# Optimization experiments

Hardware: AMD Instinct MI355X
Metric: run time of the kernel (lower is better)

The kernel has to match this reference:

```python
import jax, jax.numpy as jnp
import numpy as np

OBS_DIM = 64; ACT_DIM = 18; INTER = 64; COMMAND = 32
UNITS = ACT_DIM + COMMAND + INTER  # 114; neuron order: [motor, command, inter]
Q_HIDDEN = max(32, UNITS)
B, T = 2048, 64
ODE_UNFOLDS = 6
EPS = 1e-8


def _build_wiring(seed=0):
    """NCP sparse wiring: sensory->inter, inter->command, command recurrent, command->motor."""
    rng = np.random.default_rng(seed)
    adj = np.zeros((UNITS, UNITS), np.float32)   # [pre, post]
    sens = np.zeros((OBS_DIM, UNITS), np.float32)
    motor = np.arange(ACT_DIM)
    cmd = np.arange(ACT_DIM, ACT_DIM + COMMAND)
    inter = np.arange(ACT_DIM + COMMAND, UNITS)
    for s in range(OBS_DIM):
        for d in rng.choice(inter, size=8, replace=False):
            sens[s, d] = rng.choice([-1.0, 1.0])
    for i in inter:
        for d in rng.choice(cmd, size=8, replace=False):
            adj[i, d] = rng.choice([-1.0, 1.0])
    for _ in range(32):
        adj[rng.choice(cmd), rng.choice(cmd)] = rng.choice([-1.0, 1.0])
    for m in motor:
        for s in rng.choice(cmd, size=8, replace=False):
            adj[s, m] = rng.choice([-1.0, 1.0])
    return adj, sens


def setup_inputs() -> dict:
    key = jax.random.key(0)
    ks = jax.random.split(key, 16)
    adj, sens = _build_wiring()
    u = lambda k, shape, lo, hi: jax.random.uniform(k, shape, jnp.float32, lo, hi)
    return {
        "obs": jax.random.normal(ks[0], (B, T, OBS_DIM), jnp.float32),
        "hidden": jnp.zeros((B, UNITS), jnp.float32),
        "input_w": jnp.ones((OBS_DIM,), jnp.float32),
        "input_b": jnp.zeros((OBS_DIM,), jnp.float32),
        "sensory_w": u(ks[1], (OBS_DIM, UNITS), 0.001, 1.0),
        "sensory_mu": u(ks[2], (OBS_DIM, UNITS), 0.3, 0.8),
        "sensory_sigma": u(ks[3], (OBS_DIM, UNITS), 3.0, 8.0),
        "sensory_erev": jnp.asarray(sens),
        "sensory_mask": jnp.asarray(np.abs(sens)),
        "w": u(ks[4], (UNITS, UNITS), 0.001, 1.0),
        "mu": u(ks[5], (UNITS, UNITS), 0.3, 0.8),
        "sigma": u(ks[6], (UNITS, UNITS), 3.0, 8.0),
        "erev": jnp.asarray(adj),
        "mask": jnp.asarray(np.abs(adj)),
        "gleak": u(ks[7], (UNITS,), 0.001, 1.0),
        "vleak": u(ks[8], (UNITS,), -0.2, 0.2),
        "cm": u(ks[9], (UNITS,), 0.4, 0.6),
        "q_w1": jax.random.normal(ks[10], (UNITS, Q_HIDDEN), jnp.float32) / np.sqrt(UNITS).astype(np.float32),
        "q_b1": jnp.zeros((Q_HIDDEN,), jnp.float32),
        "q_w2": jax.random.normal(ks[11], (Q_HIDDEN, ACT_DIM), jnp.float32) / np.sqrt(Q_HIDDEN).astype(np.float32),
        "q_b2": jnp.zeros((ACT_DIM,), jnp.float32),
    }


def _ltc_forward(obs, hidden, input_w, input_b, sensory_w, sensory_mu, sensory_sigma,
                 sensory_erev, sensory_mask, w, mu, sigma, erev, mask, gleak, vleak, cm):
    sw = sensory_w * sensory_mask          # sparse sensory synapses (S, U)
    ww = w * mask                          # sparse recurrent synapses (U, U)
    cm_t = cm * ODE_UNFOLDS                # cm / (elapsed_time / ode_unfolds), elapsed_time = 1.0

    @jax.checkpoint
    def step(h, x):
        xi = x * input_w + input_b                                                    # (B, S) affine input map
        s_act = sw * jax.nn.sigmoid((xi[:, :, None] - sensory_mu) * sensory_sigma)    # (B, S, U)
        w_num_s = jnp.sum(s_act * sensory_erev, axis=1)                               # (B, U)
        w_den_s = jnp.sum(s_act, axis=1)                                              # (B, U)

        def unfold(v, _):
            act = ww * jax.nn.sigmoid((v[:, :, None] - mu) * sigma)                   # (B, U, U)
            num = cm_t * v + gleak * vleak + jnp.sum(act * erev, axis=1) + w_num_s
            den = cm_t + gleak + jnp.sum(act, axis=1) + w_den_s
            return num / (den + EPS), None

        v, _ = jax.lax.scan(unfold, h, None, length=ODE_UNFOLDS)
        return v, None

    h, _ = jax.lax.scan(step, hidden, jnp.swapaxes(obs, 0, 1))  # scan over time
    return h


def reference(obs, hidden, input_w, input_b, sensory_w, sensory_mu, sensory_sigma,
              sensory_erev, sensory_mask, w, mu, sigma, erev, mask, gleak, vleak, cm,
              q_w1, q_b1, q_w2, q_b2):
    h = _ltc_forward(obs, hidden, input_w, input_b, sensory_w, sensory_mu, sensory_sigma,
                     sensory_erev, sensory_mask, w, mu, sigma, erev, mask, gleak, vleak, cm)
    q = jax.nn.relu(h @ q_w1 + q_b1) @ q_w2 + q_b2  # Q-head over full hidden state
    return q, h
```

## Files before the change

kernel.cpp:

```cpp
#include <hip/hip_runtime.h>

#define UNITS   114
#define SDIM    64
#define ACT     18
#define TSTEPS  64

#define CR 13
#define CS 9
#define MSTRIDE 24

#define LOG2E 1.4426950408889634f
#define EPS   1e-8f

typedef float v2f __attribute__((ext_vector_type(2)));
__device__ __forceinline__ v2f fma2(v2f a, v2f b, v2f c) {
  return __builtin_elementwise_fma(a, b, c);
}
__device__ __forceinline__ float bperm(int addr, float v) {
  return __int_as_float(__builtin_amdgcn_ds_bpermute(addr, __float_as_int(v)));
}
__device__ __forceinline__ float dperm(int addr, float v) {
  return __int_as_float(__builtin_amdgcn_ds_permute(addr, __float_as_int(v)));
}
__device__ __forceinline__ void wsync() {
  __builtin_amdgcn_fence(__ATOMIC_ACQ_REL, "wavefront");
  __builtin_amdgcn_wave_barrier();
}
__device__ __forceinline__ int canonLane(int u) { return (u >= 64) ? (u - 64) : u; }

__device__ __forceinline__ int kthSetBit(unsigned long long m, int k) {
  int pos = 0;
#pragma unroll
  for (int ww = 32; ww >= 1; ww >>= 1) {
    const unsigned long long lowMask = ((1ull << ww) - 1ull);
    const int c = __popcll(m & lowMask);
    if (k >= c) { k -= c; m >>= ww; pos += ww; }
  }
  return pos;
}
__device__ __forceinline__ unsigned long long shfl_u64(unsigned long long v, int src) {
  const int lo = __shfl((int)(unsigned)(v & 0xffffffffull), src);
  const int hi = __shfl((int)(unsigned)(v >> 32), src);
  return ((unsigned long long)(unsigned)hi << 32) | (unsigned)lo;
}

__global__ __launch_bounds__(64) void build_all(
    const float* __restrict__ w,  const float* __restrict__ mu,
    const float* __restrict__ sigma, const float* __restrict__ erev,
    const float* __restrict__ mask,
    const float* __restrict__ sw, const float* __restrict__ smu,
    const float* __restrict__ ssg, const float* __restrict__ serev,
    const float* __restrict__ smask,
    float4* __restrict__ recP4, float2* __restrict__ recP2, int* __restrict__ recAd,
    float4* __restrict__ senP4, float2* __restrict__ senP2, int* __restrict__ senAd,
    int* __restrict__ meta)
{
  const int l = threadIdx.x;
  const int bid = blockIdx.x;
  __shared__ int degL[64], pF0L[64];
  __shared__ int contIdx[64], contOwn[64], splitRole[64], split2[64], ownP[128];
  __shared__ int rcv[64];

  contIdx[l] = 0; contOwn[l] = 0; splitRole[l] = -1; split2[l] = 0;
  ownP[2*l] = -1; ownP[2*l+1] = -1;

  if (bid < 4) {
    unsigned long long cLo = 0ull, cHi = 0ull;
    if (l < 50) {
      for (int base = 0; base < 64; base += 16) {
        float mv[16];
#pragma unroll
        for (int q = 0; q < 16; ++q) mv[q] = mask[(18 + base + q)*UNITS + l];
#pragma unroll
        for (int q = 0; q < 16; ++q) if (mv[q] != 0.f) cLo |= (1ull << (base + q));
      }
      for (int base = 0; base < 32; base += 16) {
        float mv[16];
#pragma unroll
        for (int q = 0; q < 16; ++q) mv[q] = mask[(82 + base + q)*UNITS + l];
#pragma unroll
        for (int q = 0; q < 16; ++q) if (mv[q] != 0.f) cHi |= (1ull << (base + q));
      }
    }
    const int dreg = __popcll(cLo) + __popcll(cHi);
    degL[l] = dreg;
    wsync();
    {
      int lam = 0, f = 0, pc = 0;
      for (int p = 0; p < 50; ++p) {
        const int dd = __shfl(dreg, p);
        if (pc == 2 || f == CR || dd > 3*CR - f) { ++lam; f = 0; pc = 0; }
        if (lam > 63) lam = 63;
        if (l == 0) { pF0L[p] = f; ownP[2*lam + pc] = p; }
        const int owner = lam, role = pc; ++pc;
        const int take = dd < (CR - f) ? dd : (CR - f);
        f += take; int rem = dd - take;
        if (rem > 0) {
          if (l == 0) { splitRole[owner] = role; split2[owner] = (rem > CR) ? 1 : 0; }
          ++lam; if (lam > 63) lam = 63;
          if (l == 0) { contIdx[lam] = 1; contOwn[lam] = owner; }
          pc = 1;
          const int t2 = rem < CR ? rem : CR; f = t2; rem -= t2;
          if (rem > 0) {
            ++lam; if (lam > 63) lam = 63;
            if (l == 0) { contIdx[lam] = 2; contOwn[lam] = owner; }
            pc = 1; f = rem;
          }
        }
      }
    }
    wsync();
    int dAr = (contIdx[l] == 1) ? contOwn[l] : -1;
    int dBr = (contIdx[l] == 2) ? contOwn[l] : -1;
    rcv[l] = 0; wsync();
    if (dAr >= 0) rcv[dAr] = 1;
    wsync();
    { const unsigned long long rM = __ballot(rcv[l] != 0), dM = __ballot(dAr < 0);
      if (dAr < 0) dAr = kthSetBit(~rM, __popcll(dM & ((1ull << l) - 1ull))); }
    wsync();
    rcv[l] = 0; wsync();
    if (dBr >= 0) rcv[dBr] = 1;
    wsync();
    { const unsigned long long rM = __ballot(rcv[l] != 0), dM = __ballot(dBr < 0);
      if (dBr < 0) dBr = kthSetBit(~rM, __popcll(dM & ((1ull << l) - 1ull))); }
    const int uA = ownP[2*l], uB = ownP[2*l+1];
    if (bid == 0) {
      int* M = meta + l * MSTRIDE;
      M[0] = dAr * 4; M[1] = dBr * 4;
      const float s1A = (splitRole[l] == 0) ? 1.f : 0.f, s1B = (splitRole[l] == 1) ? 1.f : 0.f;
      M[2] = __float_as_int(s1A); M[3] = __float_as_int(s1B);
      const float s2 = split2[l] ? 1.f : 0.f;
      M[4] = __float_as_int(s1A * s2); M[5] = __float_as_int(s1B * s2);
      M[6] = ((uA >= 0) ? uA : 128 + l) * 4;
      M[7] = ((uB >= 0) ? uB : 192 + l) * 4;
      M[8] = (uA >= 0) ? uA : 0;
      M[9] = (uB >= 0) ? uB : 0;
    }
    const int ci = contIdx[l];
    int p1 = -1, br = 0, cnt1 = 0;
    if (ci) {
      const int o = contOwn[l];
      p1 = ownP[2*o + splitRole[o]];
      br = (CR - pF0L[p1]) + ((ci == 2) ? CR : 0);
      cnt1 = degL[p1] - br; if (cnt1 > CR) cnt1 = CR;
    }
    int fA = 0, tA = -1;
    if (uA >= 0) { fA = pF0L[uA]; const int rm = CR - fA; const int dd = degL[uA]; tA = dd < rm ? dd : rm; }
    int fB = 0, tB = -1;
    if (uB >= 0) { fB = pF0L[uB]; const int rm = CR - fB; const int dd = degL[uB]; tB = dd < rm ? dd : rm; }
    for (int s = bid; s < CR; s += 4) {
      int post = -1, rank = 0, isB = 0;
      if (ci && s < cnt1)                          { post = p1; rank = br + s; }
      else if (uA >= 0 && s >= fA && s < fA + tA)  { post = uA; rank = s - fA; }
      else if (uB >= 0 && s >= fB && s < fB + tB)  { post = uB; rank = s - fB; isB = 1; }
      const int postc = (post >= 0) ? post : 0;
      const unsigned long long plo = shfl_u64(cLo, postc);
      const unsigned long long phi = shfl_u64(cHi, postc);
      float4 p4 = make_float4(0.f, 0.f, 0.f, 0.f);
      float2 p2 = make_float2(0.f, 0.f);
      int ad = 0;
      if (post >= 0) {
        const int c = __popcll(plo);
        const int pre = (rank < c) ? (18 + kthSetBit(plo, rank)) : (82 + kthSetBit(phi, rank - c));
        const int idx = pre * UNITS + post;
        const float sg_ = sigma[idx];
        const float nsgl = -sg_ * LOG2E, msl = mu[idx] * sg_ * LOG2E;
        const float wd = w[idx], wn = wd * erev[idx];
        p4 = make_float4(nsgl, msl, isB ? 0.f : wn, isB ? 0.f : wd);
        p2 = isB ? make_float2(wn, wd) : make_float2(0.f, 0.f);
        ad = pre * 4;
      }
      recP4[s*64 + l] = p4; recP2[s*64 + l] = p2; recAd[s*64 + l] = ad;
    }
  } else {
    unsigned long long cS = 0ull;
    {
      const int col = 50 + l;
      for (int base = 0; base < 64; base += 16) {
        float mv[16];
#pragma unroll
        for (int q = 0; q < 16; ++q) mv[q] = smask[(base + q)*UNITS + col];
#pragma unroll
        for (int q = 0; q < 16; ++q) if (mv[q] != 0.f) cS |= (1ull << (base + q));
      }
    }
    const int dreg = __popcll(cS);
    degL[l] = dreg;
    wsync();
    {
      int lam = 0, f = 0, pc = 0;
      for (int p = 0; p < 64; ++p) {
        const int dd = __shfl(dreg, p);
        if (pc == 2 || f == CS || dd > 3*CS - f) { ++lam; f = 0; pc = 0; }
        if (lam > 63) lam = 63;
        if (l == 0) { pF0L[p] = f; ownP[2*lam + pc] = p; }
        const int owner = lam, role = pc; ++pc;
        const int take = dd < (CS - f) ? dd : (CS - f);
        f += take; int rem = dd - take;
        if (rem > 0) {
          if (l == 0) { splitRole[owner] = role; split2[owner] = (rem > CS) ? 1 : 0; }
          ++lam; if (lam > 63) lam = 63;
          if (l == 0) { contIdx[lam] = 1; contOwn[lam] = owner; }
          pc = 1;
          const int t2 = rem < CS ? rem : CS; f = t2; rem -= t2;
          if (rem > 0) {
            ++lam; if (lam > 63) lam = 63;
            if (l == 0) { contIdx[lam] = 2; contOwn[lam] = owner; }
            pc = 1; f = rem;
          }
        }
      }
    }
    wsync();
    int dAs = (contIdx[l] == 1) ? contOwn[l] : -1;
    int dBs = (contIdx[l] == 2) ? contOwn[l] : -1;
    rcv[l] = 0; wsync();
    if (dAs >= 0) rcv[dAs] = 1;
    wsync();
    { const unsigned long long rM = __ballot(rcv[l] != 0), dM = __ballot(dAs < 0);
      if (dAs < 0) dAs = kthSetBit(~rM, __popcll(dM & ((1ull << l) - 1ull))); }
    wsync();
    rcv[l] = 0; wsync();
    if (dBs >= 0) rcv[dBs] = 1;
    wsync();
    { const unsigned long long rM = __ballot(rcv[l] != 0), dM = __ballot(dBs < 0);
      if (dBs < 0) dBs = kthSetBit(~rM, __popcll(dM & ((1ull << l) - 1ull))); }
    wsync();
    int rAs = (ownP[2*l]   >= 0) ? canonLane(50 + ownP[2*l])   : -1;
    int rBs = (ownP[2*l+1] >= 0) ? canonLane(50 + ownP[2*l+1]) : -1;
    rcv[l] = 0; wsync();
    if (rAs >= 0) rcv[rAs] = 1;
    wsync();
    const int isRcvA = rcv[l];
    { const unsigned long long rM = __ballot(isRcvA != 0), dM = __ballot(rAs < 0);
      if (rAs < 0) rAs = kthSetBit(~rM, __popcll(dM & ((1ull << l) - 1ull))); }
    wsync();
    rcv[l] = 0; wsync();
    if (rBs >= 0) rcv[rBs] = 1;
    wsync();
    { const unsigned long long rM = __ballot(rcv[l] != 0), dM = __ballot(rBs < 0);
      if (rBs < 0) rBs = kthSetBit(~rM, __popcll(dM & ((1ull << l) - 1ull))); }
    const int pAs = ownP[2*l], pBs = ownP[2*l+1];
    if (bid == 4) {
      int* M = meta + l * MSTRIDE;
      M[10] = dAs * 4; M[11] = dBs * 4;
      const float s1A = (splitRole[l] == 0) ? 1.f : 0.f, s1B = (splitRole[l] == 1) ? 1.f : 0.f;
      M[12] = __float_as_int(s1A); M[13] = __float_as_int(s1B);
      const float s2 = split2[l] ? 1.f : 0.f;
      M[14] = __float_as_int(s1A * s2); M[15] = __float_as_int(s1B * s2);
      M[16] = rAs * 4; M[17] = rBs * 4;
      M[18] = __float_as_int(isRcvA ? 1.f : 0.f);
      M[19] = __float_as_int(isRcvA ? 0.f : 1.f);
      M[20] = (pAs >= 0) ? 50 + pAs : 0;
      M[21] = (pBs >= 0) ? 50 + pBs : 0;
    }
    const int ci = contIdx[l];
    int p1 = -1, br = 0, cnt1 = 0;
    if (ci) {
      const int o = contOwn[l];
      p1 = ownP[2*o + splitRole[o]];
      br = (CS - pF0L[p1]) + ((ci == 2) ? CS : 0);
      cnt1 = degL[p1] - br; if (cnt1 > CS) cnt1 = CS;
    }
    int fA = 0, tA = -1;
    if (pAs >= 0) { fA = pF0L[pAs]; const int rm = CS - fA; const int dd = degL[pAs]; tA = dd < rm ? dd : rm; }
    int fB = 0, tB = -1;
    if (pBs >= 0) { fB = pF0L[pBs]; const int rm = CS - fB; const int dd = degL[pBs]; tB = dd < rm ? dd : rm; }
    for (int s = bid - 4; s < CS; s += 4) {
      int post = -1, rank = 0, isB = 0;
      if (ci && s < cnt1)                            { post = p1;  rank = br + s; }
      else if (pAs >= 0 && s >= fA && s < fA + tA)   { post = pAs; rank = s - fA; }
      else if (pBs >= 0 && s >= fB && s < fB + tB)   { post = pBs; rank = s - fB; isB = 1; }
      const int postc = (post >= 0) ? post : 0;
      const unsigned long long pm = shfl_u64(cS, postc);
      float4 p4 = make_float4(0.f, 0.f, 0.f, 0.f);
      float2 p2 = make_float2(0.f, 0.f);
      int ad = 0;
      if (post >= 0) {
        const int pre = kthSetBit(pm, rank);
        const int idx = pre * UNITS + 50 + post;
        const float sg_ = ssg[idx];
        const float nsgl = -sg_ * LOG2E, msl = smu[idx] * sg_ * LOG2E;
        const float wd = sw[idx], wn = wd * serev[idx];
        p4 = make_float4(nsgl, msl, isB ? 0.f : wn, isB ? 0.f : wd);
        p2 = isB ? make_float2(wn, wd) : make_float2(0.f, 0.f);
        ad = pre * 4;
      }
      senP4[s*64 + l] = p4; senP2[s*64 + l] = p2; senAd[s*64 + l] = ad;
    }
  }
}

__global__ __launch_bounds__(64, 2) void ltc_run(
    const float* __restrict__ obs,     const float* __restrict__ hidden,
    const float* __restrict__ input_w, const float* __restrict__ input_b,
    const float* __restrict__ gleak,   const float* __restrict__ vleak,
    const float* __restrict__ cm,
    const float* __restrict__ q_w1, const float* __restrict__ q_b1,
    const float* __restrict__ q_w2, const float* __restrict__ q_b2,
    const float4* __restrict__ recP4, const float2* __restrict__ recP2,
    const int* __restrict__ recAd,
    const float4* __restrict__ senP4, const float2* __restrict__ senP2,
    const int* __restrict__ senAd,
    const int* __restrict__ meta, float* __restrict__ out, int B)
{
  const int l = threadIdx.x, b = blockIdx.x;
  __shared__ float mirror[256];
  char* mbase = (char*)mirror;

  float rNS[CR], rMS[CR]; v2f rWA[CR], rWB[CR]; int rad[CR];
#pragma unroll
  for (int s = 0; s < CR; ++s) {
    const float4 p4 = recP4[s*64 + l]; const float2 p2 = recP2[s*64 + l];
    rNS[s] = p4.x; rMS[s] = p4.y; rWA[s] = (v2f){p4.z, p4.w};
    rWB[s] = (v2f){p2.x, p2.y}; rad[s] = recAd[s*64 + l];
  }
  float sNS[CS], sMS[CS]; v2f sWA[CS], sWB[CS]; int sad[CS];
#pragma unroll
  for (int s = 0; s < CS; ++s) {
    const float4 p4 = senP4[s*64 + l]; const float2 p2 = senP2[s*64 + l];
    sNS[s] = p4.x; sMS[s] = p4.y; sWA[s] = (v2f){p4.z, p4.w};
    sWB[s] = (v2f){p2.x, p2.y}; sad[s] = senAd[s*64 + l];
  }

  const int* M = meta + l * MSTRIDE;
  const int   rPush1 = M[0], rPush2 = M[1];
  const v2f gR1A = {__int_as_float(M[2]), __int_as_float(M[2])};
  const v2f gR1B = {__int_as_float(M[3]), __int_as_float(M[3])};
  const v2f gR2A = {__int_as_float(M[4]), __int_as_float(M[4])};
  const v2f gR2B = {__int_as_float(M[5]), __int_as_float(M[5])};
  const int   rWrA = M[6], rWrB = M[7], rUA = M[8], rUB = M[9];
  const int   sPush1 = M[10], sPush2 = M[11];
  const v2f gS1A = {__int_as_float(M[12]), __int_as_float(M[12])};
  const v2f gS1B = {__int_as_float(M[13]), __int_as_float(M[13])};
  const v2f gS2A = {__int_as_float(M[14]), __int_as_float(M[14])};
  const v2f gS2B = {__int_as_float(M[15]), __int_as_float(M[15])};
  const int   sRtA = M[16], sRtB = M[17];
  const float sRndA = __int_as_float(M[18]), sRndB = __int_as_float(M[19]);
  const int   sUA = M[20], sUB = M[21];

  const float cmA  = cm[rUA]*6.f, glvA  = gleak[rUA]*vleak[rUA], cgA  = cm[rUA]*6.f + gleak[rUA] + EPS;
  const float cmB  = cm[rUB]*6.f, glvB  = gleak[rUB]*vleak[rUB], cgB  = cm[rUB]*6.f + gleak[rUB] + EPS;
  const float cmSA = cm[sUA]*6.f, glvSA = gleak[sUA]*vleak[sUA], cgSA = cm[sUA]*6.f + gleak[sUA] + EPS;
  const float cmSB = cm[sUB]*6.f, glvSB = gleak[sUB]*vleak[sUB], cgSB = cm[sUB]*6.f + gleak[sUB] + EPS;

  const bool ownA  = (rWrA < 512), ownB  = (rWrB < 512);
  const bool ownSA = (sUA != 0),   ownSB = (sUB != 0);
  const v2f initRA = ownA  ? (v2f){glvA,  cgA}  : (v2f){0.f, EPS};
  const v2f initRB = ownB  ? (v2f){glvB,  cgB}  : (v2f){0.f, EPS};
  const v2f initSA = ownSA ? (v2f){glvSA, cgSA} : (v2f){0.f, EPS};
  const v2f initSB = ownSB ? (v2f){glvSB, cgSB} : (v2f){0.f, EPS};

  const int  iUnit = (l < 50) ? 64 + l : l;
  const int  iWr   = iUnit * 4;
  float vIn = hidden[(size_t)b*UNITS + iUnit];
  float vPA = hidden[(size_t)b*UNITS + rUA];
  float vPB = hidden[(size_t)b*UNITS + rUB];

  mirror[l] = hidden[(size_t)b*UNITS + l];
  if (l < 50) mirror[64 + l] = hidden[(size_t)b*UNITS + 64 + l];

  const float iw = input_w[l], ibv = input_b[l];
  const float* ob = obs + (size_t)b*(TSTEPS*SDIM) + l;

  float aI, bI;
  {
    const float xi = fmaf(ob[0], iw, ibv);
    float uu[CS];
#pragma unroll
    for (int s = 0; s < CS; ++s) {
      float z = fmaf(bperm(sad[s], xi), sNS[s], sMS[s]);
      z = fminf(z, 30.f);
      uu[s] = 1.f + __builtin_amdgcn_exp2f(z);
    }
    float sg[CS];
#pragma unroll
    for (int q = 0; q < 4; ++q) {
      const float p = uu[2*q] * uu[2*q+1];
      const float r = __builtin_amdgcn_rcpf(p);
      sg[2*q]   = uu[2*q+1] * r;
      sg[2*q+1] = uu[2*q]   * r;
    }
    sg[8] = __builtin_amdgcn_rcpf(uu[8]);
    v2f cA = {0.f,0.f}, cB = {0.f,0.f};
#pragma unroll
    for (int s = 0; s < CS; ++s) {
      const v2f s2 = {sg[s], sg[s]};
      cA = fma2(sWA[s], s2, cA);
      cB = fma2(sWB[s], s2, cB);
    }
    const v2f m1 = {dperm(sPush1, cA.x), dperm(sPush1, cA.y)};
    const v2f m2 = {dperm(sPush2, cA.x), dperm(sPush2, cA.y)};
    v2f tA = fma2(gS1A, m1, cA); tA = fma2(gS2A, m2, tA);
    v2f tB = fma2(gS1B, m1, cB); tB = fma2(gS2B, m2, tB);
    const float rdA = __builtin_amdgcn_rcpf(cgSA + tA.y);
    const float aA = cmSA * rdA, bA = (glvSA + tA.x) * rdA;
    const float rdB = __builtin_amdgcn_rcpf(cgSB + tB.y);
    const float aB = cmSB * rdB, bB = (glvSB + tB.x) * rdB;
    const float ra1 = dperm(sRtA, aA), rb1 = dperm(sRtA, bA);
    const float ra2 = dperm(sRtB, aB), rb2 = dperm(sRtB, bB);
    aI = sRndA*ra1 + sRndB*ra2;
    bI = sRndA*rb1 + sRndB*rb2;
  }

  float xiN = fmaf(ob[SDIM], iw, ibv);
  float xrC = ob[2*SDIM];
  float su[CS];
  v2f acA = initSA, acB = initSB;
  v2f tSA = {0.f,0.f}, tSB = {0.f,0.f};
  float aIn = 0.f, bIn = 0.f;

  auto unfold = [&](auto chunk) {
    wsync();
    float uu[CR];
#pragma unroll
    for (int s = 0; s < CR; ++s) {
      const float pv = *(const float*)(mbase + rad[s]);
      const float z = fmaf(pv, rNS[s], rMS[s]);
      uu[s] = 1.f + __builtin_amdgcn_exp2f(z);
    }
    chunk();
    float sg[CR];
#pragma unroll
    for (int q = 0; q < 5; ++q) {
      const float p = uu[2*q] * uu[2*q+1];
      const float r = __builtin_amdgcn_rcpf(p);
      sg[2*q]   = uu[2*q+1] * r;
      sg[2*q+1] = uu[2*q]   * r;
    }
    {
      const float p01 = uu[10]*uu[11];
      const float r = __builtin_amdgcn_rcpf(p01*uu[12]);
      const float t12 = uu[12]*r;
      sg[10] = uu[11]*t12; sg[11] = uu[10]*t12; sg[12] = p01*r;
    }
    v2f a0 = initRA, a1 = {0.f,0.f}, b0 = initRB, b1 = {0.f,0.f};
#pragma unroll
    for (int s = 0; s < CR; ++s) {
      const v2f s2 = {sg[s], sg[s]};
      if (s & 1) { a1 = fma2(rWA[s], s2, a1); b1 = fma2(rWB[s], s2, b1); }
      else       { a0 = fma2(rWA[s], s2, a0); b0 = fma2(rWB[s], s2, b0); }
    }
    v2f aA = a0 + a1, aB = b0 + b1;
    const v2f m1 = {dperm(rPush1, aA.x), dperm(rPush1, aA.y)};
    const v2f m2 = {dperm(rPush2, aA.x), dperm(rPush2, aA.y)};
    v2f tA = fma2(gR1A, m1, aA); tA = fma2(gR2A, m2, tA);
    v2f tB = fma2(gR1B, m1, aB); tB = fma2(gR2B, m2, tB);
    const float dAq = tA.y, dBq = tB.y;
    const float rr = __builtin_amdgcn_rcpf(dAq * dBq);
    vPA = fmaf(cmA, vPA, tA.x) * (dBq * rr);
    vPB = fmaf(cmB, vPB, tB.x) * (dAq * rr);
    vIn = fmaf(aI, vIn, bI);
    wsync();
    *(float*)(mbase + rWrA) = vPA;
    *(float*)(mbase + rWrB) = vPB;
    *(float*)(mbase + iWr)  = vIn;
  };

  auto sExp = [&](int s) {
    float z = fmaf(bperm(sad[s], xiN), sNS[s], sMS[s]);
    z = fminf(z, 30.f);
    su[s] = 1.f + __builtin_amdgcn_exp2f(z);
  };
  auto sPair = [&](int s0) {
    const float p = su[s0] * su[s0+1];
    const float r = __builtin_amdgcn_rcpf(p);
    const float g0 = su[s0+1] * r, g1 = su[s0] * r;
    acA = fma2(sWA[s0],   (v2f){g0,g0}, acA);
    acA = fma2(sWA[s0+1], (v2f){g1,g1}, acA);
    acB = fma2(sWB[s0],   (v2f){g0,g0}, acB);
    acB = fma2(sWB[s0+1], (v2f){g1,g1}, acB);
  };

#pragma unroll 1
  for (int t = 0; t < TSTEPS; ++t) {
    unfold([&]{ sExp(0); sExp(1); });
    unfold([&]{ sExp(2); sExp(3); sPair(0); });
    unfold([&]{ sExp(4); sExp(5); sPair(2); });
    unfold([&]{ sExp(6); sExp(7); sExp(8); sPair(4); });
    unfold([&]{
      const float p67 = su[6] * su[7];
      const float r = __builtin_amdgcn_rcpf(p67 * su[8]);
      const float t67 = su[8] * r;
      const float g6 = su[7]*t67, g7 = su[6]*t67, g8 = p67*r;
      acA = fma2(sWA[6], (v2f){g6,g6}, acA); acB = fma2(sWB[6], (v2f){g6,g6}, acB);
      acA = fma2(sWA[7], (v2f){g7,g7}, acA); acB = fma2(sWB[7], (v2f){g7,g7}, acB);
      acA = fma2(sWA[8], (v2f){g8,g8}, acA); acB = fma2(sWB[8], (v2f){g8,g8}, acB);
      const v2f m1 = {dperm(sPush1, acA.x), dperm(sPush1, acA.y)};
      const v2f m2 = {dperm(sPush2, acA.x), dperm(sPush2, acA.y)};
      tSA = fma2(gS1A, m1, acA); tSA = fma2(gS2A, m2, tSA);
      tSB = fma2(gS1B, m1, acB); tSB = fma2(gS2B, m2, tSB);
    });
    unfold([&]{
      const float dA_ = tSA.y, dB_ = tSB.y;
      const float rr = __builtin_amdgcn_rcpf(dA_ * dB_);
      const float rdA = dB_ * rr, rdB = dA_ * rr;
      const float aA = cmSA * rdA, bA = tSA.x * rdA;
      const float aB = cmSB * rdB, bB = tSB.x * rdB;
      const float ra1 = dperm(sRtA, aA), rb1 = dperm(sRtA, bA);
      const float ra2 = dperm(sRtB, aB), rb2 = dperm(sRtB, bB);
      aIn = sRndA*ra1 + sRndB*ra2;
      bIn = sRndA*rb1 + sRndB*rb2;
    });
    aI = aIn; bI = bIn;
    xiN = fmaf(xrC, iw, ibv);
    const int tn = (t + 3 < TSTEPS) ? (t + 3) : (TSTEPS - 1);
    xrC = ob[tn * SDIM];
    acA = initSA; acB = initSB;
  }
  wsync();

  float* __restrict__ outH = out + (size_t)B * ACT;
  outH[(size_t)b*UNITS + l] = mirror[l];
  if (l < 50) outH[(size_t)b*UNITS + 64 + l] = mirror[64 + l];

  const int j2 = (l < 50) ? 64 + l : l;
  float h1 = q_b1[l], h2 = q_b1[j2];
  for (int i = 0; i < UNITS; ++i) {
    const float hv = mirror[i];
    h1 = fmaf(hv, q_w1[i*UNITS + l],  h1);
    h2 = fmaf(hv, q_w1[i*UNITS + j2], h2);
  }
  h1 = fmaxf(h1, 0.f); h2 = fmaxf(h2, 0.f);
  wsync();
  mirror[l] = h1;
  if (l < 50) mirror[64 + l] = h2;
  wsync();
  if (l < ACT) {
    float q = q_b2[l];
    for (int i = 0; i < UNITS; ++i) q = fmaf(mirror[i], q_w2[i*ACT + l], q);
    out[(size_t)b*ACT + l] = q;
  }
}

extern "C" void kernel_launch(void* const* d_in, const int* in_sizes, int n_in,
                              void* d_out, int out_size, void* d_ws, size_t ws_size,
                              hipStream_t stream)
{
  const float* obs           = (const float*)d_in[0];
  const float* hidden        = (const float*)d_in[1];
  const float* input_w       = (const float*)d_in[2];
  const float* input_b       = (const float*)d_in[3];
  const float* sensory_w     = (const float*)d_in[4];
  const float* sensory_mu    = (const float*)d_in[5];
  const float* sensory_sigma = (const float*)d_in[6];
  const float* sensory_erev  = (const float*)d_in[7];
  const float* sensory_mask  = (const float*)d_in[8];
  const float* w             = (const float*)d_in[9];
  const float* mu            = (const float*)d_in[10];
  const float* sigma         = (const float*)d_in[11];
  const float* erev          = (const float*)d_in[12];
  const float* mask          = (const float*)d_in[13];
  const float* gleak         = (const float*)d_in[14];
  const float* vleak         = (const float*)d_in[15];
  const float* cm            = (const float*)d_in[16];
  const float* q_w1          = (const float*)d_in[17];
  const float* q_b1          = (const float*)d_in[18];
  const float* q_w2          = (const float*)d_in[19];
  const float* q_b2          = (const float*)d_in[20];

  char* ws = (char*)d_ws;
  float4* recP4 = (float4*)(ws);
  float2* recP2 = (float2*)(ws + 13312);
  int*    recAd = (int*)   (ws + 19968);
  float4* senP4 = (float4*)(ws + 23296);
  float2* senP2 = (float2*)(ws + 32512);
  int*    senAd = (int*)   (ws + 37120);
  int*    meta  = (int*)   (ws + 39424);

  build_all<<<8, 64, 0, stream>>>(
      w, mu, sigma, erev, mask,
      sensory_w, sensory_mu, sensory_sigma, sensory_erev, sensory_mask,
      recP4, recP2, recAd, senP4, senP2, senAd, meta);

  const int B = in_sizes[0] / (TSTEPS * SDIM);
  ltc_run<<<B, 64, 0, stream>>>(
      obs, hidden, input_w, input_b, gleak, vleak, cm,
      q_w1, q_b1, q_w2, q_b2,
      recP4, recP2, recAd, senP4, senP2, senAd, meta,
      (float*)d_out, B);
}
```

Baseline: 359.3 us.

## Split LTC recurrence across two waves with shared-memory partial sums

Each block now runs two wavefronts: the first handles 8 of the 13 recurrent synapse slots and the state update, and the second handles the remaining 5 slots plus the sensory/input pipeline, passing partial sums through shared memory. Sensory weights move from registers to LDS to reduce register pressure and allow higher occupancy. The intent is to shorten per-unfold critical-path work, at the cost of two block-level barriers per ODE unfold instead of wavefront-only syncs.

```diff
diff --git a/kernel.cpp b/kernel.cpp
--- a/kernel.cpp
+++ b/kernel.cpp
@@ -8,6 +8,9 @@
 #define CR 13
 #define CS 9
 #define MSTRIDE 24
+
+#define NR0 8
+#define NR1 (CR - NR0)
 
 #define LOG2E 1.4426950408889634f
 #define EPS   1e-8f
@@ -291,7 +294,7 @@
   }
 }
 
-__global__ __launch_bounds__(64, 2) void ltc_run(
+__global__ __launch_bounds__(128, 4) void ltc_run(
     const float* __restrict__ obs,     const float* __restrict__ hidden,
     const float* __restrict__ input_w, const float* __restrict__ input_b,
     const float* __restrict__ gleak,   const float* __restrict__ vleak,
@@ -304,232 +307,274 @@
     const int* __restrict__ senAd,
     const int* __restrict__ meta, float* __restrict__ out, int B)
 {
-  const int l = threadIdx.x, b = blockIdx.x;
+  const int tid = threadIdx.x, b = blockIdx.x, cl = tid & 63;
   __shared__ float mirror[256];
+  __shared__ float4 part[64];
+  __shared__ float4 sw4[CS*64];
   char* mbase = (char*)mirror;
 
-  float rNS[CR], rMS[CR]; v2f rWA[CR], rWB[CR]; int rad[CR];
-#pragma unroll
-  for (int s = 0; s < CR; ++s) {
-    const float4 p4 = recP4[s*64 + l]; const float2 p2 = recP2[s*64 + l];
-    rNS[s] = p4.x; rMS[s] = p4.y; rWA[s] = (v2f){p4.z, p4.w};
-    rWB[s] = (v2f){p2.x, p2.y}; rad[s] = recAd[s*64 + l];
+  if (tid < UNITS) mirror[tid] = hidden[(size_t)b*UNITS + tid];
+  for (int i = tid; i < CS*64; i += 128) {
+    const float4 p4 = senP4[i]; const float2 p2 = senP2[i];
+    sw4[i] = make_float4(p4.z, p4.w, p2.x, p2.y);
   }
-  float sNS[CS], sMS[CS]; v2f sWA[CS], sWB[CS]; int sad[CS];
-#pragma unroll
-  for (int s = 0; s < CS; ++s) {
-    const float4 p4 = senP4[s*64 + l]; const float2 p2 = senP2[s*64 + l];
-    sNS[s] = p4.x; sMS[s] = p4.y; sWA[s] = (v2f){p4.z, p4.w};
-    sWB[s] = (v2f){p2.x, p2.y}; sad[s] = senAd[s*64 + l];
-  }
-
-  const int* M = meta + l * MSTRIDE;
-  const int   rPush1 = M[0], rPush2 = M[1];
+  const int* M = meta + cl * MSTRIDE;
+  const int rPush1 = M[0], rPush2 = M[1];
   const v2f gR1A = {__int_as_float(M[2]), __int_as_float(M[2])};
   const v2f gR1B = {__int_as_float(M[3]), __int_as_float(M[3])};
   const v2f gR2A = {__int_as_float(M[4]), __int_as_float(M[4])};
   const v2f gR2B = {__int_as_float(M[5]), __int_as_float(M[5])};
-  const int   rWrA = M[6], rWrB = M[7], rUA = M[8], rUB = M[9];
-  const int   sPush1 = M[10], sPush2 = M[11];
-  const v2f gS1A = {__int_as_float(M[12]), __int_as_float(M[12])};
-  const v2f gS1B = {__int_as_float(M[13]), __int_as_float(M[13])};
-  const v2f gS2A = {__int_as_float(M[14]), __int_as_float(M[14])};
-  const v2f gS2B = {__int_as_float(M[15]), __int_as_float(M[15])};
-  const int   sRtA = M[16], sRtB = M[17];
-  const float sRndA = __int_as_float(M[18]), sRndB = __int_as_float(M[19]);
-  const int   sUA = M[20], sUB = M[21];
-
-  const float cmA  = cm[rUA]*6.f, glvA  = gleak[rUA]*vleak[rUA], cgA  = cm[rUA]*6.f + gleak[rUA] + EPS;
-  const float cmB  = cm[rUB]*6.f, glvB  = gleak[rUB]*vleak[rUB], cgB  = cm[rUB]*6.f + gleak[rUB] + EPS;
-  const float cmSA = cm[sUA]*6.f, glvSA = gleak[sUA]*vleak[sUA], cgSA = cm[sUA]*6.f + gleak[sUA] + EPS;
-  const float cmSB = cm[sUB]*6.f, glvSB = gleak[sUB]*vleak[sUB], cgSB = cm[sUB]*6.f + gleak[sUB] + EPS;
-
-  const bool ownA  = (rWrA < 512), ownB  = (rWrB < 512);
-  const bool ownSA = (sUA != 0),   ownSB = (sUB != 0);
-  const v2f initRA = ownA  ? (v2f){glvA,  cgA}  : (v2f){0.f, EPS};
-  const v2f initRB = ownB  ? (v2f){glvB,  cgB}  : (v2f){0.f, EPS};
-  const v2f initSA = ownSA ? (v2f){glvSA, cgSA} : (v2f){0.f, EPS};
-  const v2f initSB = ownSB ? (v2f){glvSB, cgSB} : (v2f){0.f, EPS};
-
-  const int  iUnit = (l < 50) ? 64 + l : l;
-  const int  iWr   = iUnit * 4;
-  float vIn = hidden[(size_t)b*UNITS + iUnit];
-  float vPA = hidden[(size_t)b*UNITS + rUA];
-  float vPB = hidden[(size_t)b*UNITS + rUB];
-
-  mirror[l] = hidden[(size_t)b*UNITS + l];
-  if (l < 50) mirror[64 + l] = hidden[(size_t)b*UNITS + 64 + l];
-
-  const float iw = input_w[l], ibv = input_b[l];
-  const float* ob = obs + (size_t)b*(TSTEPS*SDIM) + l;
-
-  float aI, bI;
-  {
-    const float xi = fmaf(ob[0], iw, ibv);
-    float uu[CS];
+  __syncthreads();
+
+  if (tid < 64) {
+    float rNS[NR0], rMS[NR0]; v2f rWA[NR0], rWB[NR0]; int rad[NR0];
+#pragma unroll
+    for (int s = 0; s < NR0; ++s) {
+      const float4 p4 = recP4[s*64 + cl]; const float2 p2 = recP2[s*64 + cl];
+      rNS[s] = p4.x; rMS[s] = p4.y; rWA[s] = (v2f){p4.z, p4.w};
+      rWB[s] = (v2f){p2.x, p2.y}; rad[s] = recAd[s*64 + cl];
+    }
+    const int rWrA = M[6], rWrB = M[7], rUA = M[8], rUB = M[9];
+    const float cmA = cm[rUA]*6.f, glvA = gleak[rUA]*vleak[rUA], cgA = cm[rUA]*6.f + gleak[rUA] + EPS;
+    const float cmB = cm[rUB]*6.f, glvB = gleak[rUB]*vleak[rUB], cgB = cm[rUB]*6.f + gleak[rUB] + EPS;
+    const bool ownA = (rWrA < 512), ownB = (rWrB < 512);
+    const v2f initRA = ownA ? (v2f){glvA, cgA} : (v2f){0.f, EPS};
+    const v2f initRB = ownB ? (v2f){glvB, cgB} : (v2f){0.f, EPS};
+    float vPA = hidden[(size_t)b*UNITS + rUA];
+    float vPB = hidden[(size_t)b*UNITS + rUB];
+
+#pragma unroll 1
+    for (int it = 0; it < TSTEPS*6; ++it) {
+      __syncthreads();
+      float uu[NR0];
+#pragma unroll
+      for (int s = 0; s < NR0; ++s) {
+        const float pv = *(const float*)(mbase + rad[s]);
+        const float z = fmaf(pv, rNS[s], rMS[s]);
+        uu[s] = 1.f + __builtin_amdgcn_exp2f(z);
+      }
+      float sg[NR0];
+#pragma unroll
+      for (int q = 0; q < NR0/2; ++q) {
+        const float p = uu[2*q] * uu[2*q+1];
+        const float r = __builtin_amdgcn_rcpf(p);
+        sg[2*q]   = uu[2*q+1] * r;
+        sg[2*q+1] = uu[2*q]   * r;
+      }
+      v2f a0 = initRA, a1 = {0.f,0.f}, b0 = initRB, b1 = {0.f,0.f};
+#pragma unroll
+      for (int s = 0; s < NR0; ++s) {
+        const v2f s2 = {sg[s], sg[s]};
+        if (s & 1) { a1 = fma2(rWA[s], s2, a1); b1 = fma2(rWB[s], s2, b1); }
+        else       { a0 = fma2(rWA[s], s2, a0); b0 = fma2(rWB[s], s2, b0); }
+      }
+      const v2f aA = a0 + a1, aB = b0 + b1;
+      const v2f m1 = {dperm(rPush1, aA.x), dperm(rPush1, aA.y)};
+      const v2f m2 = {dperm(rPush2, aA.x), dperm(rPush2, aA.y)};
+      v2f tA = fma2(gR1A, m1, aA); tA = fma2(gR2A, m2, tA);
+      v2f tB = fma2(gR1B, m1, aB); tB = fma2(gR2B, m2, tB);
+      __syncthreads();
+      const float4 pp = part[cl];
+      tA = tA + (v2f){pp.x, pp.y};
+      tB = tB + (v2f){pp.z, pp.w};
+      const float dAq = tA.y, dBq = tB.y;
+      const float rr = __builtin_amdgcn_rcpf(dAq * dBq);
+      vPA = fmaf(cmA, vPA, tA.x) * (dBq * rr);
+      vPB = fmaf(cmB, vPB, tB.x) * (dAq * rr);
+      *(float*)(mbase + rWrA) = vPA;
+      *(float*)(mbase + rWrB) = vPB;
+    }
+  } else {
+    float rNS[NR1], rMS[NR1]; v2f rWA[NR1], rWB[NR1]; int rad[NR1];
+#pragma unroll
+    for (int s = 0; s < NR1; ++s) {
+      const float4 p4 = recP4[(NR0+s)*64 + cl]; const float2 p2 = recP2[(NR0+s)*64 + cl];
+      rNS[s] = p4.x; rMS[s] = p4.y; rWA[s] = (v2f){p4.z, p4.w};
+      rWB[s] = (v2f){p2.x, p2.y}; rad[s] = recAd[(NR0+s)*64 + cl];
+    }
+    float sNS[CS], sMS[CS]; int sad[CS];
 #pragma unroll
     for (int s = 0; s < CS; ++s) {
-      float z = fmaf(bperm(sad[s], xi), sNS[s], sMS[s]);
-      z = fminf(z, 30.f);
-      uu[s] = 1.f + __builtin_amdgcn_exp2f(z);
-    }
-    float sg[CS];
-#pragma unroll
-    for (int q = 0; q < 4; ++q) {
-      const float p = uu[2*q] * uu[2*q+1];
-      const float r = __builtin_amdgcn_rcpf(p);
-      sg[2*q]   = uu[2*q+1] * r;
-      sg[2*q+1] = uu[2*q]   * r;
-    }
-    sg[8] = __builtin_amdgcn_rcpf(uu[8]);
-    v2f cA = {0.f,0.f}, cB = {0.f,0.f};
-#pragma unroll
-    for (int s = 0; s < CS; ++s) {
-      const v2f s2 = {sg[s], sg[s]};
-      cA = fma2(sWA[s], s2, cA);
-      cB = fma2(sWB[s], s2, cB);
-    }
-    const v2f m1 = {dperm(sPush1, cA.x), dperm(sPush1, cA.y)};
-    const v2f m2 = {dperm(sPush2, cA.x), dperm(sPush2, cA.y)};
-    v2f tA = fma2(gS1A, m1, cA); tA = fma2(gS2A, m2, tA);
-    v2f tB = fma2(gS1B, m1, cB); tB = fma2(gS2B, m2, tB);
-    const float rdA = __builtin_amdgcn_rcpf(cgSA + tA.y);
-    const float aA = cmSA * rdA, bA = (glvSA + tA.x) * rdA;
-    const float rdB = __builtin_amdgcn_rcpf(cgSB + tB.y);
-    const float aB = cmSB * rdB, bB = (glvSB + tB.x) * rdB;
-    const float ra1 = dperm(sRtA, aA), rb1 = dperm(sRtA, bA);
-    const float ra2 = dperm(sRtB, aB), rb2 = dperm(sRtB, bB);
-    aI = sRndA*ra1 + sRndB*ra2;
-    bI = sRndA*rb1 + sRndB*rb2;
-  }
-
-  float xiN = fmaf(ob[SDIM], iw, ibv);
-  float xrC = ob[2*SDIM];
-  float su[CS];
-  v2f acA = initSA, acB = initSB;
-  v2f tSA = {0.f,0.f}, tSB = {0.f,0.f};
-  float aIn = 0.f, bIn = 0.f;
-
-  auto unfold = [&](auto chunk) {
-    wsync();
-    float uu[CR];
-#pragma unroll
-    for (int s = 0; s < CR; ++s) {
-      const float pv = *(const float*)(mbase + rad[s]);
-      const float z = fmaf(pv, rNS[s], rMS[s]);
-      uu[s] = 1.f + __builtin_amdgcn_exp2f(z);
-    }
-    chunk();
-    float sg[CR];
-#pragma unroll
-    for (int q = 0; q < 5; ++q) {
-      const float p = uu[2*q] * uu[2*q+1];
-      const float r = __builtin_amdgcn_rcpf(p);
-      sg[2*q]   = uu[2*q+1] * r;
-      sg[2*q+1] = uu[2*q]   * r;
-    }
+      const float4 p4 = senP4[s*64 + cl];
+      sNS[s] = p4.x; sMS[s] = p4.y; sad[s] = senAd[s*64 + cl];
+    }
+    const int sPush1 = M[10], sPush2 = M[11];
+    const v2f gS1A = {__int_as_float(M[12]), __int_as_float(M[12])};
+    const v2f gS1B = {__int_as_float(M[13]), __int_as_float(M[13])};
+    const v2f gS2A = {__int_as_float(M[14]), __int_as_float(M[14])};
+    const v2f gS2B = {__int_as_float(M[15]), __int_as_float(M[15])};
+    const int sRtA = M[16], sRtB = M[17];
+    const float sRndA = __int_as_float(M[18]), sRndB = __int_as_float(M[19]);
+    const int sUA = M[20], sUB = M[21];
+    const float cmSA = cm[sUA]*6.f, glvSA = gleak[sUA]*vleak[sUA], cgSA = cm[sUA]*6.f + gleak[sUA] + EPS;
+    const float cmSB = cm[sUB]*6.f, glvSB = gleak[sUB]*vleak[sUB], cgSB = cm[sUB]*6.f + gleak[sUB] + EPS;
+    const bool ownSA = (sUA != 0), ownSB = (sUB != 0);
+    const v2f initSA = ownSA ? (v2f){glvSA, cgSA} : (v2f){0.f, EPS};
+    const v2f initSB = ownSB ? (v2f){glvSB, cgSB} : (v2f){0.f, EPS};
+    const int iUnit = (cl < 50) ? 64 + cl : cl;
+    const int iWr = iUnit * 4;
+    float vIn = hidden[(size_t)b*UNITS + iUnit];
+    const float iw = input_w[cl], ibv = input_b[cl];
+    const float* ob = obs + (size_t)b*(TSTEPS*SDIM) + cl;
+
+    float aI, bI;
     {
-      const float p01 = uu[10]*uu[11];
-      const float r = __builtin_amdgcn_rcpf(p01*uu[12]);
-      const float t12 = uu[12]*r;
-      sg[10] = uu[11]*t12; sg[11] = uu[10]*t12; sg[12] = p01*r;
-    }
-    v2f a0 = initRA, a1 = {0.f,0.f}, b0 = initRB, b1 = {0.f,0.f};
-#pragma unroll
-    for (int s = 0; s < CR; ++s) {
-      const v2f s2 = {sg[s], sg[s]};
-      if (s & 1) { a1 = fma2(rWA[s], s2, a1); b1 = fma2(rWB[s], s2, b1); }
-      else       { a0 = fma2(rWA[s], s2, a0); b0 = fma2(rWB[s], s2, b0); }
-    }
-    v2f aA = a0 + a1, aB = b0 + b1;
-    const v2f m1 = {dperm(rPush1, aA.x), dperm(rPush1, aA.y)};
-    const v2f m2 = {dperm(rPush2, aA.x), dperm(rPush2, aA.y)};
-    v2f tA = fma2(gR1A, m1, aA); tA = fma2(gR2A, m2, tA);
-    v2f tB = fma2(gR1B, m1, aB); tB = fma2(gR2B, m2, tB);
-    const float dAq = tA.y, dBq = tB.y;
-    const float rr = __builtin_amdgcn_rcpf(dAq * dBq);
-    vPA = fmaf(cmA, vPA, tA.x) * (dBq * rr);
-    vPB = fmaf(cmB, vPB, tB.x) * (dAq * rr);
-    vIn = fmaf(aI, vIn, bI);
-    wsync();
-    *(float*)(mbase + rWrA) = vPA;
-    *(float*)(mbase + rWrB) = vPB;
-    *(float*)(mbase + iWr)  = vIn;
-  };
-
-  auto sExp = [&](int s) {
-    float z = fmaf(bperm(sad[s], xiN), sNS[s], sMS[s]);
-    z = fminf(z, 30.f);
-    su[s] = 1.f + __builtin_amdgcn_exp2f(z);
-  };
-  auto sPair = [&](int s0) {
-    const float p = su[s0] * su[s0+1];
-    const float r = __builtin_amdgcn_rcpf(p);
-    const float g0 = su[s0+1] * r, g1 = su[s0] * r;
-    acA = fma2(sWA[s0],   (v2f){g0,g0}, acA);
-    acA = fma2(sWA[s0+1], (v2f){g1,g1}, acA);
-    acB = fma2(sWB[s0],   (v2f){g0,g0}, acB);
-    acB = fma2(sWB[s0+1], (v2f){g1,g1}, acB);
-  };
-
-#pragma unroll 1
-  for (int t = 0; t < TSTEPS; ++t) {
-    unfold([&]{ sExp(0); sExp(1); });
-    unfold([&]{ sExp(2); sExp(3); sPair(0); });
-    unfold([&]{ sExp(4); sExp(5); sPair(2); });
-    unfold([&]{ sExp(6); sExp(7); sExp(8); sPair(4); });
-    unfold([&]{
-      const float p67 = su[6] * su[7];
-      const float r = __builtin_amdgcn_rcpf(p67 * su[8]);
-      const float t67 = su[8] * r;
-      const float g6 = su[7]*t67, g7 = su[6]*t67, g8 = p67*r;
-      acA = fma2(sWA[6], (v2f){g6,g6}, acA); acB = fma2(sWB[6], (v2f){g6,g6}, acB);
-      acA = fma2(sWA[7], (v2f){g7,g7}, acA); acB = fma2(sWB[7], (v2f){g7,g7}, acB);
-      acA = fma2(sWA[8], (v2f){g8,g8}, acA); acB = fma2(sWB[8], (v2f){g8,g8}, acB);
-      const v2f m1 = {dperm(sPush1, acA.x), dperm(sPush1, acA.y)};
-      const v2f m2 = {dperm(sPush2, acA.x), dperm(sPush2, acA.y)};
-      tSA = fma2(gS1A, m1, acA); tSA = fma2(gS2A, m2, tSA);
-      tSB = fma2(gS1B, m1, acB); tSB = fma2(gS2B, m2, tSB);
-    });
-    unfold([&]{
-      const float dA_ = tSA.y, dB_ = tSB.y;
-      const float rr = __builtin_amdgcn_rcpf(dA_ * dB_);
-      const float rdA = dB_ * rr, rdB = dA_ * rr;
-      const float aA = cmSA * rdA, bA = tSA.x * rdA;
-      const float aB = cmSB * rdB, bB = tSB.x * rdB;
+      const float xi = fmaf(ob[0], iw, ibv);
+      float uu[CS];
+#pragma unroll
+      for (int s = 0; s < CS; ++s) {
+        float z = fmaf(bperm(sad[s], xi), sNS[s], sMS[s]);
+        z = fminf(z, 30.f);
+        uu[s] = 1.f + __builtin_amdgcn_exp2f(z);
+      }
+      float sg[CS];
+#pragma unroll
+      for (int q = 0; q < 4; ++q) {
+        const float p = uu[2*q] * uu[2*q+1];
+        const float r = __builtin_amdgcn_rcpf(p);
+        sg[2*q]   = uu[2*q+1] * r;
+        sg[2*q+1] = uu[2*q]   * r;
+      }
+      sg[8] = __builtin_amdgcn_rcpf(uu[8]);
+      v2f cA = {0.f,0.f}, cB = {0.f,0.f};
+#pragma unroll
+      for (int s = 0; s < CS; ++s) {
+        const float4 wz = sw4[s*64 + cl];
+        const v2f s2 = {sg[s], sg[s]};
+        cA = fma2((v2f){wz.x, wz.y}, s2, cA);
+        cB = fma2((v2f){wz.z, wz.w}, s2, cB);
+      }
+      const v2f m1 = {dperm(sPush1, cA.x), dperm(sPush1, cA.y)};
+      const v2f m2 = {dperm(sPush2, cA.x), dperm(sPush2, cA.y)};
+      v2f tA = fma2(gS1A, m1, cA); tA = fma2(gS2A, m2, tA);
+      v2f tB = fma2(gS1B, m1, cB); tB = fma2(gS2B, m2, tB);
+      const float rdA = __builtin_amdgcn_rcpf(cgSA + tA.y);
+      const float aA = cmSA * rdA, bA = (glvSA + tA.x) * rdA;
+      const float rdB = __builtin_amdgcn_rcpf(cgSB + tB.y);
+      const float aB = cmSB * rdB, bB = (glvSB + tB.x) * rdB;
       const float ra1 = dperm(sRtA, aA), rb1 = dperm(sRtA, bA);
       const float ra2 = dperm(sRtB, aB), rb2 = dperm(sRtB, bB);
-      aIn = sRndA*ra1 + sRndB*ra2;
-      bIn = sRndA*rb1 + sRndB*rb2;
-    });
-    aI = aIn; bI = bIn;
-    xiN = fmaf(xrC, iw, ibv);
-    const int tn = (t + 3 < TSTEPS) ? (t + 3) : (TSTEPS - 1);
-    xrC = ob[tn * SDIM];
-    acA = initSA; acB = initSB;
+      aI = sRndA*ra1 + sRndB*ra2;
+      bI = sRndA*rb1 + sRndB*rb2;
+    }
+
+    float xiN = fmaf(ob[SDIM], iw, ibv);
+    float xrC = ob[2*SDIM];
+    float su[CS];
+    v2f acA = initSA, acB = initSB;
+    v2f tSA = {0.f,0.f}, tSB = {0.f,0.f};
+    float aIn = 0.f, bIn = 0.f;
+
+    auto recHalf = [&]{
+      float uu[NR1];
+#pragma unroll
+      for (int s = 0; s < NR1; ++s) {
+        const float pv = *(const float*)(mbase + rad[s]);
+        const float z = fmaf(pv, rNS[s], rMS[s]);
+        uu[s] = 1.f + __builtin_amdgcn_exp2f(z);
+      }
+      float sg[NR1];
+#pragma unroll
+      for (int q = 0; q < NR1/2; ++q) {
+        const float p = uu[2*q] * uu[2*q+1];
+        const float r = __builtin_amdgcn_rcpf(p);
+        sg[2*q]   = uu[2*q+1] * r;
+        sg[2*q+1] = uu[2*q]   * r;
+      }
+      sg[NR1-1] = __builtin_amdgcn_rcpf(uu[NR1-1]);
+      v2f a0 = {0.f,0.f}, a1 = {0.f,0.f}, b0 = {0.f,0.f}, b1 = {0.f,0.f};
+#pragma unroll
+      for (int s = 0; s < NR1; ++s) {
+        const v2f s2 = {sg[s], sg[s]};
+        if (s & 1) { a1 = fma2(rWA[s], s2, a1); b1 = fma2(rWB[s], s2, b1); }
+        else       { a0 = fma2(rWA[s], s2, a0); b0 = fma2(rWB[s], s2, b0); }
+      }
+      const v2f pA = a0 + a1, pB = b0 + b1;
+      const v2f m1 = {dperm(rPush1, pA.x), dperm(rPush1, pA.y)};
+      const v2f m2 = {dperm(rPush2, pA.x), dperm(rPush2, pA.y)};
+      v2f cA = fma2(gR1A, m1, pA); cA = fma2(gR2A, m2, cA);
+      v2f cB = fma2(gR1B, m1, pB); cB = fma2(gR2B, m2, cB);
+      part[cl] = make_float4(cA.x, cA.y, cB.x, cB.y);
+    };
+    auto sExp = [&](int s) {
+      float z = fmaf(bperm(sad[s], xiN), sNS[s], sMS[s]);
+      z = fminf(z, 30.f);
+      su[s] = 1.f + __builtin_amdgcn_exp2f(z);
+    };
+    auto sPair = [&](int s0) {
+      const float p = su[s0] * su[s0+1];
+      const float r = __builtin_amdgcn_rcpf(p);
+      const float g0 = su[s0+1] * r, g1 = su[s0] * r;
+      const float4 wa = sw4[s0*64 + cl], wb = sw4[(s0+1)*64 + cl];
+      acA = fma2((v2f){wa.x, wa.y}, (v2f){g0,g0}, acA);
+      acB = fma2((v2f){wa.z, wa.w}, (v2f){g0,g0}, acB);
+      acA = fma2((v2f){wb.x, wb.y}, (v2f){g1,g1}, acA);
+      acB = fma2((v2f){wb.z, wb.w}, (v2f){g1,g1}, acB);
+    };
+    auto phase = [&](auto chunk) {
+      __syncthreads();
+      recHalf();
+      __syncthreads();
+      vIn = fmaf(aI, vIn, bI);
+      *(float*)(mbase + iWr) = vIn;
+      chunk();
+    };
+
+#pragma unroll 1
+    for (int t = 0; t < TSTEPS; ++t) {
+      phase([&]{ sExp(0); sExp(1); });
+      phase([&]{ sExp(2); sExp(3); sPair(0); });
+      phase([&]{ sExp(4); sExp(5); sPair(2); });
+      phase([&]{ sExp(6); sExp(7); sExp(8); sPair(4); });
+      phase([&]{
+        const float p67 = su[6] * su[7];
+        const float r = __builtin_amdgcn_rcpf(p67 * su[8]);
+        const float t67 = su[8] * r;
+        const float g6 = su[7]*t67, g7 = su[6]*t67, g8 = p67*r;
+        const float4 w6 = sw4[6*64 + cl], w7 = sw4[7*64 + cl], w8 = sw4[8*64 + cl];
+        acA = fma2((v2f){w6.x,w6.y}, (v2f){g6,g6}, acA); acB = fma2((v2f){w6.z,w6.w}, (v2f){g6,g6}, acB);
+        acA = fma2((v2f){w7.x,w7.y}, (v2f){g7,g7}, acA); acB = fma2((v2f){w7.z,w7.w}, (v2f){g7,g7}, acB);
+        acA = fma2((v2f){w8.x,w8.y}, (v2f){g8,g8}, acA); acB = fma2((v2f){w8.z,w8.w}, (v2f){g8,g8}, acB);
+        const v2f m1 = {dperm(sPush1, acA.x), dperm(sPush1, acA.y)};
+        const v2f m2 = {dperm(sPush2, acA.x), dperm(sPush2, acA.y)};
+        tSA = fma2(gS1A, m1, acA); tSA = fma2(gS2A, m2, tSA);
+        tSB = fma2(gS1B, m1, acB); tSB = fma2(gS2B, m2, tSB);
+      });
+      phase([&]{
+        const float dA_ = tSA.y, dB_ = tSB.y;
+        const float rr = __builtin_amdgcn_rcpf(dA_ * dB_);
+        const float rdA = dB_ * rr, rdB = dA_ * rr;
+        const float aA = cmSA * rdA, bA = tSA.x * rdA;
+        const float aB = cmSB * rdB, bB = tSB.x * rdB;
+        const float ra1 = dperm(sRtA, aA), rb1 = dperm(sRtA, bA);
+        const float ra2 = dperm(sRtB, aB), rb2 = dperm(sRtB, bB);
+        aIn = sRndA*ra1 + sRndB*ra2;
+        bIn = sRndA*rb1 + sRndB*rb2;
+      });
+      aI = aIn; bI = bIn;
+      xiN = fmaf(xrC, iw, ibv);
+      const int tn = (t + 3 < TSTEPS) ? (t + 3) : (TSTEPS - 1);
+      xrC = ob[tn * SDIM];
+      acA = initSA; acB = initSB;
+    }
   }
-  wsync();
+  __syncthreads();
 
   float* __restrict__ outH = out + (size_t)B * ACT;
-  outH[(size_t)b*UNITS + l] = mirror[l];
-  if (l < 50) outH[(size_t)b*UNITS + 64 + l] = mirror[64 + l];
-
-  const int j2 = (l < 50) ? 64 + l : l;
-  float h1 = q_b1[l], h2 = q_b1[j2];
-  for (int i = 0; i < UNITS; ++i) {
-    const float hv = mirror[i];
-    h1 = fmaf(hv, q_w1[i*UNITS + l],  h1);
-    h2 = fmaf(hv, q_w1[i*UNITS + j2], h2);
+  if (tid < UNITS) outH[(size_t)b*UNITS + tid] = mirror[tid];
+  float h = 0.f;
+  if (tid < UNITS) {
+    h = q_b1[tid];
+    for (int i = 0; i < UNITS; ++i) h = fmaf(mirror[i], q_w1[i*UNITS + tid], h);
+    h = fmaxf(h, 0.f);
   }
-  h1 = fmaxf(h1, 0.f); h2 = fmaxf(h2, 0.f);
-  wsync();
-  mirror[l] = h1;
-  if (l < 50) mirror[64 + l] = h2;
-  wsync();
-  if (l < ACT) {
-    float q = q_b2[l];
-    for (int i = 0; i < UNITS; ++i) q = fmaf(mirror[i], q_w2[i*ACT + l], q);
-    out[(size_t)b*ACT + l] = q;
+  __syncthreads();
+  if (tid < UNITS) mirror[tid] = h;
+  __syncthreads();
+  if (tid < ACT) {
+    float q = q_b2[tid];
+    for (int i = 0; i < UNITS; ++i) q = fmaf(mirror[i], q_w2[i*ACT + tid], q);
+    out[(size_t)b*ACT + tid] = q;
   }
 }
 
@@ -574,7 +619,7 @@
       recP4, recP2, recAd, senP4, senP2, senAd, meta);
 
   const int B = in_sizes[0] / (TSTEPS * SDIM);
-  ltc_run<<<B, 64, 0, stream>>>(
+  ltc_run<<<B, 128, 0, stream>>>(
       obs, hidden, input_w, input_b, gleak, vleak, cm,
       q_w1, q_b1, q_w2, q_b2,
       recP4, recP2, recAd, senP4, senP2, senAd, meta,
```

After: 407.1 us. 13.3% more time.
